# Performance work log

Measured on AMD Instinct MI355X. Metric: run time of the kernel, lower is better.

Reference implementation:

```python
import jax, jax.numpy as jnp
import numpy as np

N, E, D, H, O = 50000, 1_600_000, 128, 64, 128
BN_EPS = 1e-5


def setup_inputs() -> dict:
    key = jax.random.key(0)
    ks = jax.random.split(key, 8)
    feat = jax.random.normal(ks[0], (N, D), dtype=jnp.float32)
    src = jax.random.randint(ks[1], (E,), 0, N, dtype=jnp.int32)
    dst = jax.random.randint(ks[2], (E,), 0, N, dtype=jnp.int32)
    s = 1.0 / np.sqrt(D)
    gamma = jnp.ones((D,), jnp.float32)
    beta = jnp.zeros((D,), jnp.float32)
    Wq = (jax.random.normal(ks[3], (D, H), dtype=jnp.float32) * s)
    bq = jnp.zeros((H,), jnp.float32)
    Wk = (jax.random.normal(ks[4], (D, H), dtype=jnp.float32) * s)
    Wv = (jax.random.normal(ks[5], (D, O), dtype=jnp.float32) * s)
    we = (jax.random.normal(ks[6], (H,), dtype=jnp.float32) / np.sqrt(H))
    return {"feat": feat, "gamma": gamma, "beta": beta, "Wq": Wq, "bq": bq,
            "Wk": Wk, "Wv": Wv, "we": we, "src": src, "dst": dst}


def reference(feat, gamma, beta, Wq, bq, Wk, Wv, we, src, dst):
    n = feat.shape[0]
    # BatchNorm1d (training-style: batch mean, biased variance)
    mean = feat.mean(axis=0)
    var = feat.var(axis=0)
    x = (feat - mean) * jax.lax.rsqrt(var + BN_EPS) * gamma + beta
    # node projections
    q = x @ Wq + bq          # [N, H]
    k = x @ Wk               # [N, H]
    v = x @ Wv               # [N, O]
    # u_add_v + fc_e(sigmoid(.)): per-edge score  [E]
    e = jax.nn.sigmoid(q[src] + k[dst]) @ we
    # edge_softmax grouped by destination node
    m = jax.ops.segment_max(e, dst, num_segments=n)
    ex = jnp.exp(e - m[dst])
    denom = jax.ops.segment_sum(ex, dst, num_segments=n)
    a = ex / denom[dst]      # [E]
    # u_mul_e_sum: weighted scatter-sum aggregation  [N, O]
    rst = jax.ops.segment_sum(v[src] * a[:, None], dst, num_segments=n)
    return rst
```

## Files before the change

### kernel.cpp

```cpp
#include <hip/hip_runtime.h>
#include <hip/hip_bf16.h>
#include <math.h>

#define BN_EPS 1e-5f
#define PGRID 256
#define CAP 96
#define CAPB 9216

typedef unsigned int u32;
typedef unsigned short u16;
typedef __attribute__((ext_vector_type(8))) short short8;
typedef __attribute__((ext_vector_type(4))) float floatx4;

__device__ __forceinline__ float bf_lo(u32 u) { return __uint_as_float(u << 16); }
__device__ __forceinline__ float bf_hi(u32 u) { return __uint_as_float(u & 0xffff0000u); }
__device__ __forceinline__ u32 bfpair(float lo, float hi) {
  u32 a = __float_as_uint(lo); a += 0x7fffu + ((a >> 16) & 1);
  u32 b = __float_as_uint(hi); b += 0x7fffu + ((b >> 16) & 1);
  return (a >> 16) | (b & 0xffff0000u);
}
__device__ __forceinline__ float sigm(float x) {
  return __builtin_amdgcn_rcpf(1.f + __expf(-x));
}

__global__ __launch_bounds__(256) void k1_stats_part_pack(
    const float* __restrict__ feat, float* __restrict__ colsum, float* __restrict__ colsq, long total,
    const int* __restrict__ src, const int* __restrict__ dst,
    int* __restrict__ bcur, u32* __restrict__ pbuf, int E, int epb, int nbuck,
    const float* __restrict__ Wq, const float* __restrict__ Wk, const float* __restrict__ Wv,
    u32* __restrict__ wt) {
  int tid = threadIdx.x;
  int bid = blockIdx.x;
  if (bid < 256) {
    long g0 = (long)bid * 256 + tid;
    float s = 0.f, sq = 0.f;
    for (long g = g0; g < total; g += 65536) { float x = feat[g]; s += x; sq += x * x; }
    __shared__ float ls[256], lq[256];
    ls[tid] = s; lq[tid] = sq;
    __syncthreads();
    if (tid < 128) {
      atomicAdd(&colsum[tid], ls[tid] + ls[tid + 128]);
      atomicAdd(&colsq[tid],  lq[tid] + lq[tid + 128]);
    }
  } else if (bid < 256 + PGRID) {
    int p = bid - 256;
    int lo = p * epb;
    int hi = lo + epb; if (hi > E) hi = E;
    __shared__ int bc_l[256], gb_l[256], cur_l[256];
    bc_l[tid] = 0;
    __syncthreads();
    for (int i = lo + tid; i < hi; i += 256)
      atomicAdd(&bc_l[dst[i] >> 8], 1);
    __syncthreads();
    if (tid < nbuck && bc_l[tid] > 0) gb_l[tid] = atomicAdd(&bcur[tid], bc_l[tid]);
    cur_l[tid] = 0;
    __syncthreads();
    for (int i = lo + tid; i < hi; i += 256) {
      int d = dst[i], s = src[i];
      int b = d >> 8;
      int r = gb_l[b] + atomicAdd(&cur_l[b], 1);
      if (r < CAPB) pbuf[(size_t)b * CAPB + r] = ((u32)(d & 255) << 16) | (u32)s;
    }
  } else {
    int col = tid;
    for (int dp = 0; dp < 64; ++dp) {
      int d = dp * 2;
      float lo, hi;
      if (col < 64)       { lo = Wq[d * 64 + col];        hi = Wq[(d + 1) * 64 + col]; }
      else if (col < 128) { lo = Wk[d * 64 + col - 64];   hi = Wk[(d + 1) * 64 + col - 64]; }
      else                { lo = Wv[d * 128 + col - 128]; hi = Wv[(d + 1) * 128 + col - 128]; }
      u32 byte = (u32)col * 256 + (u32)d * 2;
      byte ^= (u32)(col & 7) << 4;
      wt[byte >> 2] = bfpair(lo, hi);
    }
  }
}

__global__ __launch_bounds__(256) void k2_qkv_group(
    const float* __restrict__ feat, const float* __restrict__ colsum, const float* __restrict__ colsq,
    const float* __restrict__ gamma, const float* __restrict__ beta, const float* __restrict__ bq,
    const u32* __restrict__ wt,
    __hip_bfloat16* __restrict__ qbuf, float* __restrict__ kbuf, __hip_bfloat16* __restrict__ vbuf,
    int N, float invN, int QBn,
    const int* __restrict__ bcur, const u32* __restrict__ pbuf,
    int* __restrict__ cnt, u16* __restrict__ esrc) {
  int tid = threadIdx.x;
  __shared__ u32 wlds[16384];
  __shared__ float sc_lds[128], sh_lds[128];
  if ((int)blockIdx.x >= QBn) {
    int b = (int)blockIdx.x - QBn;
    int nbase = b * 256;
    int* hcur = (int*)wlds;
    hcur[tid] = 0;
    __syncthreads();
    int bc = bcur[b]; if (bc > CAPB) bc = CAPB;
    const u32* pb = pbuf + (size_t)b * CAPB;
    for (int i = tid; i < bc; i += 256) {
      u32 e = pb[i];
      int d = e >> 16, s = e & 0xffff;
      int r = atomicAdd(&hcur[d], 1);
      if (r < CAP) esrc[(size_t)(nbase + d) * CAP + r] = (u16)s;
    }
    __syncthreads();
    int nid = nbase + tid;
    if (nid < N) cnt[nid] = hcur[tid];
    return;
  }
  {
    const uint4* wg = (const uint4*)wt;
    uint4* wl = (uint4*)wlds;
#pragma unroll
    for (int i = 0; i < 16; ++i) wl[tid + i * 256] = wg[tid + i * 256];
  }
  if (tid < 128) {
    float mean = colsum[tid] * invN;
    float var  = colsq[tid] * invN - mean * mean;
    float inv  = rsqrtf(var + BN_EPS);
    float s    = gamma[tid] * inv;
    sc_lds[tid] = s; sh_lds[tid] = beta[tid] - mean * s;
  }
  __syncthreads();
  int lane = tid & 63, wv = tid >> 6;
  int arow = blockIdx.x * 64 + wv * 16 + (lane & 15);
  int kb16 = lane >> 4;
  const float* frow = feat + (long)(arow < N ? arow : N - 1) * 128;
  u32 afr[4][4];
#pragma unroll
  for (int kk = 0; kk < 4; ++kk) {
    int d0 = kk * 32 + kb16 * 8;
    float4 x0 = *(const float4*)(frow + d0);
    float4 x1 = *(const float4*)(frow + d0 + 4);
    float4 s0 = *(const float4*)&sc_lds[d0];
    float4 s1 = *(const float4*)&sc_lds[d0 + 4];
    float4 h0 = *(const float4*)&sh_lds[d0];
    float4 h1 = *(const float4*)&sh_lds[d0 + 4];
    float n0 = fmaf(x0.x, s0.x, h0.x), n1 = fmaf(x0.y, s0.y, h0.y);
    float n2 = fmaf(x0.z, s0.z, h0.z), n3 = fmaf(x0.w, s0.w, h0.w);
    float n4 = fmaf(x1.x, s1.x, h1.x), n5 = fmaf(x1.y, s1.y, h1.y);
    float n6 = fmaf(x1.z, s1.z, h1.z), n7 = fmaf(x1.w, s1.w, h1.w);
    afr[kk][0] = bfpair(n0, n1); afr[kk][1] = bfpair(n2, n3);
    afr[kk][2] = bfpair(n4, n5); afr[kk][3] = bfpair(n6, n7);
  }
  floatx4 acc[16];
#pragma unroll
  for (int ct = 0; ct < 16; ++ct) acc[ct] = (floatx4){0.f, 0.f, 0.f, 0.f};
#pragma unroll
  for (int kk = 0; kk < 4; ++kk) {
    union { u32 u[4]; short8 s; } au;
    au.u[0] = afr[kk][0]; au.u[1] = afr[kk][1]; au.u[2] = afr[kk][2]; au.u[3] = afr[kk][3];
#pragma unroll
    for (int ct = 0; ct < 16; ++ct) {
      int col = ct * 16 + (lane & 15);
      u32 byte = ((u32)col * 256 + (u32)(kk * 64 + kb16 * 16)) ^ ((u32)(col & 7) << 4);
      union { uint4 u4; short8 s; } bu;
      bu.u4 = *(const uint4*)((const char*)wlds + byte);
      acc[ct] = __builtin_amdgcn_mfma_f32_16x16x32_bf16(au.s, bu.s, acc[ct], 0, 0, 0);
    }
  }
  int crow0 = blockIdx.x * 64 + wv * 16 + (lane >> 4) * 4;
#pragma unroll
  for (int ct = 0; ct < 16; ++ct) {
    int col = ct * 16 + (lane & 15);
    float bqc = (ct < 4) ? bq[col] : 0.f;
#pragma unroll
    for (int i = 0; i < 4; ++i) {
      int row = crow0 + i;
      if (row < N) {
        float val = acc[ct][i];
        if (ct < 4)      qbuf[row * 64 + col] = __float2bfloat16(val + bqc);
        else if (ct < 8) kbuf[row * 64 + col - 64] = val;
        else             vbuf[row * 128 + col - 128] = __float2bfloat16(val);
      }
    }
  }
}

__global__ __launch_bounds__(256) void node_kernel(
    const __hip_bfloat16* __restrict__ qbt, const float* __restrict__ kb,
    const __hip_bfloat16* __restrict__ vbt, const float* __restrict__ we,
    const int* __restrict__ cnt, const u16* __restrict__ esrc,
    float* __restrict__ out, int N) {
  int tid = threadIdx.x;
  int lane = tid & 63, wvi = tid >> 6;
  int n = blockIdx.x * 4 + wvi;
  if (n >= N) return;
  int g8 = lane >> 3, hq = lane & 7;
  int deg = cnt[n]; if (deg > CAP) deg = CAP;
  int base = n * CAP;
  const uint4* qb4 = (const uint4*)qbt;
  const u32* vb32 = (const u32*)vbt;
  float4 ka  = ((const float4*)(kb + n * 64))[hq * 2];
  float4 kc  = ((const float4*)(kb + n * 64))[hq * 2 + 1];
  float4 wa  = ((const float4*)we)[hq * 2];
  float4 wb  = ((const float4*)we)[hq * 2 + 1];
  float dsum = 0.f, ax = 0.f, ay = 0.f;
  int sreg = (lane < deg) ? (int)esrc[base + lane] : 0;
  for (int cs = 0; cs < deg; cs += 64) {
    int cn = deg - cs; if (cn > 64) cn = 64;
    int rem = deg - cs - 64;
    int snext = (rem > 0 && lane < rem) ? (int)esrc[base + cs + 64 + lane] : 0;
    int nr = (cn + 7) >> 3;
    int sj0 = __shfl(sreg, g8, 64);
    uint4 qv = qb4[sj0 * 8 + hq];
    for (int r = 0; r < nr; ++r) {
      uint4 qnext;
      if (r + 1 < nr) {
        int sjn = __shfl(sreg, (r + 1) * 8 + g8, 64);
        qnext = qb4[sjn * 8 + hq];
      }
      float p;
      p  = wa.x * sigm(bf_lo(qv.x) + ka.x);
      p += wa.y * sigm(bf_hi(qv.x) + ka.y);
      p += wa.z * sigm(bf_lo(qv.y) + ka.z);
      p += wa.w * sigm(bf_hi(qv.y) + ka.w);
      p += wb.x * sigm(bf_lo(qv.z) + kc.x);
      p += wb.y * sigm(bf_hi(qv.z) + kc.y);
      p += wb.z * sigm(bf_lo(qv.w) + kc.z);
      p += wb.w * sigm(bf_hi(qv.w) + kc.w);
      p += __shfl_xor(p, 1, 64);
      p += __shfl_xor(p, 2, 64);
      p += __shfl_xor(p, 4, 64);
      int eidx = r * 8 + g8;
      float wgt = (eidx < cn) ? __expf(p) : 0.f;
      dsum += wgt;
#pragma unroll
      for (int jj = 0; jj < 8; ++jj) {
        float wj = __shfl(wgt, jj * 8, 64);
        int s2 = __shfl(sreg, r * 8 + jj, 64);
        u32 vp = vb32[s2 * 64 + lane];
        ax = fmaf(wj, bf_lo(vp), ax);
        ay = fmaf(wj, bf_hi(vp), ay);
      }
      if (r + 1 < nr) qv = qnext;
    }
    sreg = snext;
  }
  dsum += __shfl_xor(dsum, 8, 64);
  dsum += __shfl_xor(dsum, 16, 64);
  dsum += __shfl_xor(dsum, 32, 64);
  float2 r = make_float2(0.f, 0.f);
  if (deg > 0) {
    float iv = __builtin_amdgcn_rcpf(dsum);
    r.x = ax * iv; r.y = ay * iv;
  }
  ((float2*)out)[n * 64 + lane] = r;
}

extern "C" void kernel_launch(void* const* d_in, const int* in_sizes, int n_in,
                              void* d_out, int out_size, void* d_ws, size_t ws_size,
                              hipStream_t stream) {
  const float* feat  = (const float*)d_in[0];
  const float* gamma = (const float*)d_in[1];
  const float* beta  = (const float*)d_in[2];
  const float* Wq    = (const float*)d_in[3];
  const float* bq    = (const float*)d_in[4];
  const float* Wk    = (const float*)d_in[5];
  const float* Wv    = (const float*)d_in[6];
  const float* we    = (const float*)d_in[7];
  const int*   src   = (const int*)d_in[8];
  const int*   dst   = (const int*)d_in[9];
  float* out = (float*)d_out;

  const int N  = in_sizes[0] / 128;
  const int E  = in_sizes[8];
  const int QB = (N + 63) / 64;
  const int NBUCK = (N + 255) / 256;
  const int EPB = (E + PGRID - 1) / PGRID;

  char* ws = (char*)d_ws;
  size_t off = 0;
  auto alloc = [&](size_t bytes) { char* p = ws + off; off = (off + bytes + 511) & ~(size_t)511; return p; };
  float* colsum = (float*)alloc(128 * 4);
  float* colsq  = (float*)alloc(128 * 4);
  int*   bcur   = (int*)alloc((size_t)NBUCK * 4);
  u32*   wt     = (u32*)alloc(16384 * 4);
  __hip_bfloat16* qb = (__hip_bfloat16*)alloc((size_t)N * 64 * 2);
  float*          kb = (float*)alloc((size_t)N * 64 * 4);
  __hip_bfloat16* vb = (__hip_bfloat16*)alloc((size_t)N * 128 * 2);
  int* cnt  = (int*)alloc((size_t)N * 4);
  u16* esrc = (u16*)alloc((size_t)N * CAP * 2);
  u32* pbuf = (u32*)alloc((size_t)NBUCK * CAPB * 4);

  hipMemsetAsync(colsum, 0, 1024, stream);
  hipMemsetAsync(bcur, 0, (size_t)NBUCK * 4, stream);

  k1_stats_part_pack<<<256 + PGRID + 1, 256, 0, stream>>>(
      feat, colsum, colsq, (long)N * 128, src, dst, bcur, pbuf, E, EPB, NBUCK, Wq, Wk, Wv, wt);
  k2_qkv_group<<<QB + NBUCK, 256, 0, stream>>>(
      feat, colsum, colsq, gamma, beta, bq, wt, qb, kb, vb, N, 1.0f / (float)N, QB,
      bcur, pbuf, cnt, esrc);
  node_kernel<<<(N + 3) / 4, 256, 0, stream>>>(qb, kb, vb, we, cnt, esrc, out, N);
}
```

Measured before the change: 153.5 us.

## Split edge scoring and value aggregation, stage weights in LDS, widen value loads

The node kernel now runs in two phases per chunk of edges. First it computes all edge scores and stores each edge's softmax weight and source index in per-wave shared memory. Then a separate aggregation loop has each half-wave gather one edge's value row with 8-byte loads, so two edges are processed per iteration, and the halves are combined with one shuffle at the end. This removes the per-edge broadcast shuffles and the narrow 4-byte value gathers. In exchange, the q gathers are no longer interleaved with the v gathers, so latency overlap may drop. It also relies on same-wave ordering of LDS accesses without a barrier.

```diff
diff --git a/kernel.cpp b/kernel.cpp
--- a/kernel.cpp
+++ b/kernel.cpp
@@ -182,23 +182,28 @@
     float* __restrict__ out, int N) {
   int tid = threadIdx.x;
   int lane = tid & 63, wvi = tid >> 6;
+  __shared__ float wl_lds[4][64];
+  __shared__ int   sl_lds[4][64];
   int n = blockIdx.x * 4 + wvi;
   if (n >= N) return;
   int g8 = lane >> 3, hq = lane & 7;
+  int l32 = lane & 31, ehalf = lane >> 5;
   int deg = cnt[n]; if (deg > CAP) deg = CAP;
   int base = n * CAP;
   const uint4* qb4 = (const uint4*)qbt;
-  const u32* vb32 = (const u32*)vbt;
+  const uint2* vb2 = (const uint2*)vbt;
   float4 ka  = ((const float4*)(kb + n * 64))[hq * 2];
   float4 kc  = ((const float4*)(kb + n * 64))[hq * 2 + 1];
   float4 wa  = ((const float4*)we)[hq * 2];
   float4 wb  = ((const float4*)we)[hq * 2 + 1];
-  float dsum = 0.f, ax = 0.f, ay = 0.f;
+  float dsum = 0.f;
+  float a0 = 0.f, a1 = 0.f, a2 = 0.f, a3 = 0.f;
   int sreg = (lane < deg) ? (int)esrc[base + lane] : 0;
   for (int cs = 0; cs < deg; cs += 64) {
     int cn = deg - cs; if (cn > 64) cn = 64;
     int rem = deg - cs - 64;
     int snext = (rem > 0 && lane < rem) ? (int)esrc[base + cs + 64 + lane] : 0;
+    sl_lds[wvi][lane] = sreg;
     int nr = (cn + 7) >> 3;
     int sj0 = __shfl(sreg, g8, 64);
     uint4 qv = qb4[sj0 * 8 + hq];
@@ -223,27 +228,37 @@
       int eidx = r * 8 + g8;
       float wgt = (eidx < cn) ? __expf(p) : 0.f;
       dsum += wgt;
-#pragma unroll
-      for (int jj = 0; jj < 8; ++jj) {
-        float wj = __shfl(wgt, jj * 8, 64);
-        int s2 = __shfl(sreg, r * 8 + jj, 64);
-        u32 vp = vb32[s2 * 64 + lane];
-        ax = fmaf(wj, bf_lo(vp), ax);
-        ay = fmaf(wj, bf_hi(vp), ay);
-      }
+      if (hq == 0) wl_lds[wvi][eidx] = wgt;
       if (r + 1 < nr) qv = qnext;
+    }
+#pragma unroll 4
+    for (int j0 = 0; j0 < cn; j0 += 2) {
+      int j = j0 + ehalf;
+      float wj = wl_lds[wvi][j];
+      int s2   = sl_lds[wvi][j];
+      uint2 vp = vb2[s2 * 32 + l32];
+      a0 = fmaf(wj, bf_lo(vp.x), a0);
+      a1 = fmaf(wj, bf_hi(vp.x), a1);
+      a2 = fmaf(wj, bf_lo(vp.y), a2);
+      a3 = fmaf(wj, bf_hi(vp.y), a3);
     }
     sreg = snext;
   }
   dsum += __shfl_xor(dsum, 8, 64);
   dsum += __shfl_xor(dsum, 16, 64);
   dsum += __shfl_xor(dsum, 32, 64);
-  float2 r = make_float2(0.f, 0.f);
-  if (deg > 0) {
-    float iv = __builtin_amdgcn_rcpf(dsum);
-    r.x = ax * iv; r.y = ay * iv;
-  }
-  ((float2*)out)[n * 64 + lane] = r;
+  a0 += __shfl_xor(a0, 32, 64);
+  a1 += __shfl_xor(a1, 32, 64);
+  a2 += __shfl_xor(a2, 32, 64);
+  a3 += __shfl_xor(a3, 32, 64);
+  if (lane < 32) {
+    float4 o = make_float4(0.f, 0.f, 0.f, 0.f);
+    if (deg > 0) {
+      float iv = __builtin_amdgcn_rcpf(dsum);
+      o = make_float4(a0 * iv, a1 * iv, a2 * iv, a3 * iv);
+    }
+    ((float4*)out)[n * 32 + l32] = o;
+  }
 }
 
 extern "C" void kernel_launch(void* const* d_in, const int* in_sizes, int n_in,
```

New measurement: 158.8 us. +3.5%, slower.
